# Optimization experiments

Measured on AMD Instinct MI355X. Metric: run time of the kernel, lower is better.

Reference implementation:

```python
import jax, jax.numpy as jnp
import numpy as np

B, N, D = 8, 1024, 256
H = 8
DH = D // H
R = 4          # relation types 0..3; adj value 4 = no relation
FF = 1024
EPS = 1e-5


def _lin(k, fan_in, shape):
    return jax.random.normal(k, shape, jnp.float32) * (1.0 / np.sqrt(fan_in))


def setup_inputs() -> dict:
    key = jax.random.key(0)
    ks = jax.random.split(key, 16)
    src = jax.random.normal(ks[0], (B, N, D), jnp.float32)
    adj_matrix = jax.random.randint(ks[1], (B, N, N), 0, 5, dtype=jnp.int32)
    Wq = _lin(ks[2], D, (D, D)); bq = jnp.zeros((D,), jnp.float32)
    Wk = _lin(ks[3], D, (D, D)); bk = jnp.zeros((D,), jnp.float32)
    Wv = _lin(ks[4], D, (R, D, D)); bv = jnp.zeros((R, D), jnp.float32)
    Wo = _lin(ks[5], D, (D, D)); bo = jnp.zeros((D,), jnp.float32)
    W1 = _lin(ks[6], D, (D, FF)); b1 = jnp.zeros((FF,), jnp.float32)
    W2 = _lin(ks[7], FF, (FF, D)); b2 = jnp.zeros((D,), jnp.float32)
    g1 = jnp.ones((D,), jnp.float32); beta1 = jnp.zeros((D,), jnp.float32)
    g2 = jnp.ones((D,), jnp.float32); beta2 = jnp.zeros((D,), jnp.float32)
    return dict(src=src, adj_matrix=adj_matrix, Wq=Wq, bq=bq, Wk=Wk, bk=bk,
                Wv=Wv, bv=bv, Wo=Wo, bo=bo, W1=W1, b1=b1, W2=W2, b2=b2,
                g1=g1, beta1=beta1, g2=g2, beta2=beta2)


def _ln(x, g, b):
    m = x.mean(-1, keepdims=True)
    v = ((x - m) ** 2).mean(-1, keepdims=True)
    return (x - m) * jax.lax.rsqrt(v + EPS) * g + b


def reference(src, adj_matrix, Wq, bq, Wk, bk, Wv, bv, Wo, bo, W1, b1, W2, b2, g1, beta1, g2, beta2):
    Bb, Nn, Dm = src.shape
    h, dh = H, Dm // H
    q = (src @ Wq + bq).reshape(Bb, Nn, h, dh).transpose(0, 2, 1, 3)  # (B,H,N,dh)
    k = (src @ Wk + bk).reshape(Bb, Nn, h, dh).transpose(0, 2, 1, 3)
    scores = jnp.einsum('bhid,bhjd->bhij', q, k) / np.sqrt(dh)
    attn = jax.nn.softmax(scores, axis=-1)                             # (B,H,N,N)
    out = jnp.zeros_like(q)
    for r in range(Wv.shape[0]):  # small fixed relation loop, matches module
        v_r = (src @ Wv[r] + bv[r]).reshape(Bb, Nn, h, dh).transpose(0, 2, 1, 3)
        mask = (adj_matrix == r)[:, None]                              # (B,1,N,N)
        out = out + jnp.einsum('bhij,bhjd->bhid', attn * mask, v_r)
    attn_out = out.transpose(0, 2, 1, 3).reshape(Bb, Nn, Dm) @ Wo + bo
    x = _ln(src + attn_out, g1, beta1)
    ff = jax.nn.gelu(x @ W1 + b1, approximate=False) @ W2 + b2
    return _ln(x + ff, g2, beta2)
```

## Files before the change

kernel.cpp:

```cpp
#include <hip/hip_runtime.h>
#include <hip/hip_bf16.h>
#include <cmath>

constexpr int CB  = 8;
constexpr int CN  = 1024;
constexpr int CD  = 256;
constexpr int CH  = 8;
constexpr int CDH = 32;
constexpr int CR  = 4;
constexpr int CFF = 1024;
constexpr float CEPS = 1e-5f;
constexpr float CS = 0.25503480f;
constexpr size_t SZH = (size_t)CB * CH * CN * CDH;

#define MODE_QK    0
#define MODE_FFN1  2
#define MODE_VT    4

typedef float v4f __attribute__((ext_vector_type(4)));
typedef short v8s __attribute__((ext_vector_type(8)));

static __device__ __forceinline__ short f2bf(float f) {
    unsigned u = __builtin_bit_cast(unsigned, f);
    u += 0x7fff + ((u >> 16) & 1);
    return (short)(u >> 16);
}
static __device__ __forceinline__ float bf2f(short s) {
    unsigned u = ((unsigned)(unsigned short)s) << 16;
    return __builtin_bit_cast(float, u);
}
static __device__ __forceinline__ unsigned cvtpk_bf16(float lo, float hi) {
    unsigned r;
    asm("v_cvt_pk_bf16_f32 %0, %1, %2" : "=v"(r) : "v"(lo), "v"(hi));
    return r;
}

static __device__ __forceinline__ void async_copy16(const void* g, void* l) {
    __builtin_amdgcn_global_load_lds(
        (const __attribute__((address_space(1))) void*)g,
        (__attribute__((address_space(3))) void*)l, 16, 0, 0);
}


template<int BM, int BN, int MODE>
__device__ __forceinline__ void gemm_body(
    const short* __restrict__ A, const short* __restrict__ Bw,
    const float* __restrict__ biasv, void* __restrict__ dest,
    int M, int K, int Nw, int bx, int by, short* smem)
{
    constexpr int WTM = BM / 2, WTN = BN / 2;
    constexpr int TM = WTM / 16, TN = WTN / 16;
    short* As = smem;
    short* Bs = smem + 2 * BM * 32;

    const int t    = threadIdx.x;
    const int lane = t & 63;
    const int w    = t >> 6;
    const int quad = lane >> 4, l15 = lane & 15;
    const int wm = w >> 1, wn = w & 1;
    const int m0 = bx * BM, n0 = by * BN;

    const int srow = lane >> 2;
    const int scol = (lane & 3) * 8;

    v4f acc[TM][TN];
    #pragma unroll
    for (int i = 0; i < TM; ++i)
        #pragma unroll
        for (int j = 0; j < TN; ++j) acc[i][j] = (v4f){0.f, 0.f, 0.f, 0.f};

    const int NK = K >> 5;

    auto stage = [&](int buf, int kt) {
        #pragma unroll
        for (int u = 0; u < BM / 64; ++u) {
            const int e0 = (w * (BM / 64) + u) * 512;
            const int row = (e0 >> 5) + srow;
            async_copy16(A + (size_t)(m0 + row) * K + kt + scol,
                         &As[buf * BM * 32 + e0]);
        }
        #pragma unroll
        for (int u = 0; u < BN / 64; ++u) {
            const int e0 = (w * (BN / 64) + u) * 512;
            const int row = (e0 >> 5) + srow;
            async_copy16(Bw + (size_t)(n0 + row) * K + kt + scol,
                         &Bs[buf * BN * 32 + e0]);
        }
    };

    stage(0, 0);

    for (int it = 0; it < NK; ++it) {
        __syncthreads();
        if (it + 1 < NK) stage((it + 1) & 1, (it + 1) << 5);

        const int buf = it & 1;
        v8s af[TM], bfr[TN];
        #pragma unroll
        for (int i = 0; i < TM; ++i)
            af[i] = *(const v8s*)&As[buf * BM * 32 +
                                     (wm * WTM + i * 16 + l15) * 32 + quad * 8];
        #pragma unroll
        for (int j = 0; j < TN; ++j)
            bfr[j] = *(const v8s*)&Bs[buf * BN * 32 +
                                      (wn * WTN + j * 16 + l15) * 32 + quad * 8];
        #pragma unroll
        for (int i = 0; i < TM; ++i)
            #pragma unroll
            for (int j = 0; j < TN; ++j)
                acc[i][j] = __builtin_amdgcn_mfma_f32_16x16x32_bf16(
                    af[i], bfr[j], acc[i][j], 0, 0, 0);
    }

    #pragma unroll
    for (int i = 0; i < TM; ++i) {
        #pragma unroll
        for (int j = 0; j < TN; ++j) {
            const int mb = m0 + wm * WTM + i * 16 + quad * 4;
            const int n  = n0 + wn * WTN + j * 16 + l15;
            float vals[4];
            if (MODE == MODE_VT) {
                #pragma unroll
                for (int rr = 0; rr < 4; ++rr) vals[rr] = acc[i][j][rr] + biasv[mb + rr];
            } else {
                #pragma unroll
                for (int rr = 0; rr < 4; ++rr) vals[rr] = acc[i][j][rr] + biasv[n];
            }

            if (MODE == MODE_QK) {
                if (n0 < 256) {
                    #pragma unroll
                    for (int rr = 0; rr < 4; ++rr) vals[rr] *= CS;
                }
                const int b = mb >> 10, ii0 = mb & 1023;
                const int plane = n >> 8, nn = n & 255;
                const int h = nn >> 5, d = nn & 31;
                #pragma unroll
                for (int rr = 0; rr < 4; ++rr)
                    ((short*)dest)[(size_t)plane * SZH +
                        (((size_t)(b * CH + h)) * CN + ii0 + rr) * CDH + d] =
                        f2bf(vals[rr]);
            } else if (MODE == MODE_VT) {
                const int b = n >> 10, ii = n & 1023;
                const int jj = ii & 63;
                const int cc = (((jj >> 4) & 1) << 5) | (((jj >> 2) & 3) << 3) |
                               (((jj >> 5) & 1) << 2) | (jj & 3);
                const int iip = (ii & ~63) | cc;
                #pragma unroll
                for (int rr = 0; rr < 4; ++rr) {
                    const int m = mb + rr;
                    const int r2 = m >> 8, hd = m & 255;
                    const int h = hd >> 5, d = hd & 31;
                    ((short*)dest)[2 * SZH +
                        (((size_t)(r2 * 64 + b * CH + h)) * CDH + d) * CN + iip] =
                        f2bf(vals[rr]);
                }
            } else {
                #pragma unroll
                for (int rr = 0; rr < 4; ++rr) {
                    const size_t idx = (size_t)(mb + rr) * Nw + n;
                    const float xx = vals[rr];
                    const float E = exp2f(2.302217f * (xx + 0.044715f * xx * xx * xx));
                    ((short*)dest)[idx] = f2bf(xx * E / (E + 1.f));
                }
            }
        }
    }
}

template<int BM, int BN, int MODE>
__global__ __launch_bounds__(256)
void gemm_mfma(const short* __restrict__ A, const short* __restrict__ Bw,
               const float* __restrict__ biasv, void* __restrict__ dest,
               int M, int K, int Nw)
{
    extern __shared__ short smem[];
    gemm_body<BM, BN, MODE>(A, Bw, biasv, dest, M, K, Nw,
                            blockIdx.x, blockIdx.y, smem);
}

__global__ __launch_bounds__(256)
void proj_kernel(const short* __restrict__ src_bf, const short* __restrict__ wqkvT,
                 const float* __restrict__ bpack, short* __restrict__ qkv,
                 const int* __restrict__ adj, unsigned char* __restrict__ adj4)
{
    extern __shared__ short smem[];
    const int g = blockIdx.x;
    if (g < 512) {
        gemm_body<64, 128, MODE_QK>(src_bf, wqkvT, bpack, qkv,
                                    8192, 256, 512, g >> 2, g & 3, smem);
    } else if (g < 1536) {
        const int h2 = g - 512;
        gemm_body<64, 128, MODE_VT>(wqkvT + 512 * 256, src_bf, bpack + 512,
                                    qkv, 1024, 256, 8192, h2 & 15, h2 >> 4, smem);
    } else {
        const int nout = CB * CN * CN / 8;
        for (int i = (g - 1536) * 256 + threadIdx.x; i < nout; i += 512 * 256) {
            const int dwi = i & 127;
            const int row = i >> 7;
            const int T   = dwi >> 3, kq = dwi & 7;
            const int j0  = T * 64 + (kq & 3) * 4 + (kq >> 2) * 16;
            const int* p = adj + (size_t)row * CN + j0;
            const int4 q0 = *(const int4*)(p);
            const int4 q1 = *(const int4*)(p + 32);
            const unsigned pk =
                (unsigned)(q0.x & 0xf)         | ((unsigned)(q0.y & 0xf) << 4)  |
                ((unsigned)(q0.z & 0xf) << 8)  | ((unsigned)(q0.w & 0xf) << 12) |
                ((unsigned)(q1.x & 0xf) << 16) | ((unsigned)(q1.y & 0xf) << 20) |
                ((unsigned)(q1.z & 0xf) << 24) | ((unsigned)(q1.w & 0xf) << 28);
            ((unsigned*)adj4)[i] = pk;
        }
    }
}

template<bool OUTF, bool OUTB, bool ADDBF>
__global__ __launch_bounds__(256)
void gemm_ln32(const short* __restrict__ A, const short* __restrict__ Bw,
               const float* __restrict__ biasv, const void* __restrict__ addp,
               const float* __restrict__ gw, const float* __restrict__ be,
               float* __restrict__ outf, short* __restrict__ outb, int K)
{
    __shared__ short As[2][16 * 32];
    __shared__ short Bs[2][256 * 32];
    __shared__ float redS[16][4], redQ[16][4];

    const int t    = threadIdx.x;
    const int lane = t & 63;
    const int w    = t >> 6;
    const int quad = lane >> 4, l15 = lane & 15;
    const int m0   = blockIdx.x * 16;

    const int srow = lane >> 2;
    const int scol = (lane & 3) * 8;

    v4f acc[4];
    #pragma unroll
    for (int j = 0; j < 4; ++j) acc[j] = (v4f){0.f, 0.f, 0.f, 0.f};

    const int NK = K >> 5;

    auto stage = [&](int buf, int kt) {
        if (t < 64)
            async_copy16(A + (size_t)(m0 + (t >> 2)) * K + kt + (t & 3) * 8,
                         &As[buf][t * 8]);
        #pragma unroll
        for (int u = 0; u < 4; ++u) {
            const int e0 = (w * 4 + u) * 512;
            async_copy16(Bw + (size_t)((e0 >> 5) + srow) * K + kt + scol,
                         &Bs[buf][e0]);
        }
    };

    stage(0, 0);

    for (int it = 0; it < NK; ++it) {
        __syncthreads();
        if (it + 1 < NK) stage((it + 1) & 1, (it + 1) << 5);

        const int buf = it & 1;
        const v8s af = *(const v8s*)&As[buf][l15 * 32 + quad * 8];
        #pragma unroll
        for (int j = 0; j < 4; ++j) {
            const v8s bfr = *(const v8s*)&Bs[buf][(w * 64 + 16 * j + l15) * 32 + quad * 8];
            acc[j] = __builtin_amdgcn_mfma_f32_16x16x32_bf16(af, bfr, acc[j], 0, 0, 0);
        }
    }

    float v[4][4];
    #pragma unroll
    for (int rr = 0; rr < 4; ++rr) {
        const int row = m0 + quad * 4 + rr;
        float s = 0.f, sq = 0.f;
        #pragma unroll
        for (int j = 0; j < 4; ++j) {
            const int n = w * 64 + 16 * j + l15;
            const size_t idx = (size_t)row * CD + n;
            const float addv = ADDBF ? bf2f(((const short*)addp)[idx])
                                     : ((const float*)addp)[idx];
            const float x = acc[j][rr] + biasv[n] + addv;
            v[rr][j] = x;
            s += x; sq += x * x;
        }
        #pragma unroll
        for (int off = 1; off < 16; off <<= 1) {
            s  += __shfl_xor(s, off);
            sq += __shfl_xor(sq, off);
        }
        if (l15 == 0) {
            redS[quad * 4 + rr][w] = s;
            redQ[quad * 4 + rr][w] = sq;
        }
    }
    __syncthreads();

    #pragma unroll
    for (int rr = 0; rr < 4; ++rr) {
        const int r16 = quad * 4 + rr;
        const int row = m0 + r16;
        const float s  = (redS[r16][0] + redS[r16][1]) + (redS[r16][2] + redS[r16][3]);
        const float sq = (redQ[r16][0] + redQ[r16][1]) + (redQ[r16][2] + redQ[r16][3]);
        const float mean = s * (1.f / CD);
        const float var  = sq * (1.f / CD) - mean * mean;
        const float rstd = rsqrtf(var + CEPS);
        #pragma unroll
        for (int j = 0; j < 4; ++j) {
            const int n = w * 64 + 16 * j + l15;
            const float y = (v[rr][j] - mean) * rstd * gw[n] + be[n];
            if (OUTF) outf[(size_t)row * CD + n] = y;
            if (OUTB) outb[(size_t)row * CD + n] = f2bf(y);
        }
    }
}

__global__ __launch_bounds__(256)
void prep(const float* __restrict__ src,
          const float* __restrict__ Wq, const float* __restrict__ Wk,
          const float* __restrict__ Wv, const float* __restrict__ Wo,
          const float* __restrict__ W1, const float* __restrict__ W2,
          const float* __restrict__ bq, const float* __restrict__ bk,
          const float* __restrict__ bv, const float* __restrict__ bo,
          const float* __restrict__ b1, const float* __restrict__ b2,
          short* __restrict__ src_bf,
          short* __restrict__ wqkvT, short* __restrict__ woT,
          short* __restrict__ w1T, short* __restrict__ w2T,
          float* __restrict__ bpack)
{
    __shared__ float tile[64][65];
    const int bx = blockIdx.x, t = threadIdx.x;
    if (bx < 2048) {
        const int i = bx * 256 + t;
        const float4 v = ((const float4*)src)[i];
        short4 o;
        o.x = f2bf(v.x); o.y = f2bf(v.y); o.z = f2bf(v.z); o.w = f2bf(v.w);
        ((short4*)src_bf)[i] = o;
    } else if (bx < 2288) {
        const int tt = bx - 2048;
        const float* S; short* D;
        int Sstride, Dstride, k0, srccol, dstrow;
        if (tt < 96) {
            const int tk = tt & 3, tn = tt >> 2;
            const int ng = tn * 64;
            Sstride = 256; Dstride = 256; k0 = tk * 64;
            dstrow = tn * 64; D = wqkvT;
            if (ng < 256)      { S = Wq; srccol = ng; }
            else if (ng < 512) { S = Wk; srccol = ng - 256; }
            else { const int r = (ng - 512) >> 8;
                   S = Wv + (size_t)r * 65536; srccol = (ng - 512) & 255; }
        } else if (tt < 112) {
            const int u = tt - 96, tk = u & 3, tn = u >> 2;
            S = Wo; Sstride = 256; D = woT; Dstride = 256;
            k0 = tk * 64; srccol = tn * 64; dstrow = tn * 64;
        } else if (tt < 176) {
            const int u = tt - 112, tk = u & 3, tn = u >> 2;
            S = W1; Sstride = 1024; D = w1T; Dstride = 256;
            k0 = tk * 64; srccol = tn * 64; dstrow = tn * 64;
        } else {
            const int u = tt - 176, tk = u & 15, tn = u >> 4;
            S = W2; Sstride = 256; D = w2T; Dstride = 1024;
            k0 = tk * 64; srccol = tn * 64; dstrow = tn * 64;
        }
        #pragma unroll
        for (int u2 = 0; u2 < 4; ++u2) {
            const int kl = (t >> 4) + u2 * 16;
            const int nl = (t & 15) * 4;
            const float4 v = *(const float4*)&S[(size_t)(k0 + kl) * Sstride + srccol + nl];
            tile[kl][nl + 0] = v.x; tile[kl][nl + 1] = v.y;
            tile[kl][nl + 2] = v.z; tile[kl][nl + 3] = v.w;
        }
        __syncthreads();
        #pragma unroll
        for (int u2 = 0; u2 < 4; ++u2) {
            const int nl = (t >> 4) + u2 * 16;
            const int kl = (t & 15) * 4;
            short4 o;
            o.x = f2bf(tile[kl + 0][nl]); o.y = f2bf(tile[kl + 1][nl]);
            o.z = f2bf(tile[kl + 2][nl]); o.w = f2bf(tile[kl + 3][nl]);
            *(short4*)&D[(size_t)(dstrow + nl) * Dstride + k0 + kl] = o;
        }
    } else {
        const int idx = (bx - 2288) * 256 + t;
        float bvv;
        if (idx < 256)       bvv = bq[idx];
        else if (idx < 512)  bvv = bk[idx - 256];
        else if (idx < 1536) bvv = bv[idx - 512];
        else if (idx < 1792) bvv = bo[idx - 1536];
        else if (idx < 2816) bvv = b1[idx - 1792];
        else                 bvv = b2[idx - 2816];
        bpack[idx] = bvv;
    }
}

__global__ __launch_bounds__(256, 4)
void attn_mfma(const short* __restrict__ qg, const short* __restrict__ kg,
               const short* __restrict__ vt, const unsigned char* __restrict__ adj4,
               short* __restrict__ outh)
{
    __shared__ __align__(16) short vtl[2][8192];

    const int t    = threadIdx.x;
    const int lane = t & 63;
    const int w    = t >> 6;
    const int quad = lane >> 4;
    const int l15  = lane & 15;
    const int g    = blockIdx.x;
    const int b    = g & 7;
    const int h    = (g >> 3) & 7;
    const int i0   = (g >> 6) * 64;
    const int bhh  = b * CH + h;
    const size_t bh = (size_t)bhh;

    const v8s qfrag = *(const v8s*)&qg[(bh * CN + i0 + 16 * w + l15) * CDH + quad * 8];

    const short* vsrc[4];
    #pragma unroll
    for (int u = 0; u < 4; ++u) {
        const int gl = t + 256 * u;
        const int r = gl >> 8, d = (gl >> 3) & 31, gc = gl & 7;
        vsrc[u] = vt + ((size_t)(r * 64 + bhh) * CDH + d) * CN + (gc ^ (d & 7)) * 8;
    }
    const short* kbase = kg + (bh * CN + l15) * CDH + quad * 8;
    const unsigned char* abase =
        adj4 + ((size_t)(b * CN) + i0 + 16 * w + l15) * (CN / 2) + quad * 4;

    v4f oacc[2];
    oacc[0] = (v4f){0.f, 0.f, 0.f, 0.f};
    oacc[1] = (v4f){0.f, 0.f, 0.f, 0.f};
    float plsum = 0.f;
    const int psw = (l15 & 7) * 8;

    #pragma unroll
    for (int u = 0; u < 4; ++u)
        async_copy16(vsrc[u], &vtl[0][(t + 256 * u) * 8]);
    v8s kpre[4];
    #pragma unroll
    for (int jb = 0; jb < 4; ++jb)
        kpre[jb] = *(const v8s*)(kbase + (16 * jb) * CDH);
    unsigned apre0 = *(const unsigned*)(abase);
    unsigned apre1 = *(const unsigned*)(abase + 16);

    for (int jt = 0; jt < 16; ++jt) {
        __syncthreads();
        const int p = jt & 1;

        v4f sacc[4];
        #pragma unroll
        for (int jb = 0; jb < 4; ++jb)
            sacc[jb] = __builtin_amdgcn_mfma_f32_16x16x32_bf16(
                kpre[jb], qfrag, (v4f){0.f, 0.f, 0.f, 0.f}, 0, 0, 0);

        const unsigned a0 = apre0, a1 = apre1;
        const int jn = (jt + 1) & 15;
        #pragma unroll
        for (int u = 0; u < 4; ++u)
            async_copy16(vsrc[u] + jn * 64, &vtl[p ^ 1][(t + 256 * u) * 8]);
        #pragma unroll
        for (int jb = 0; jb < 4; ++jb)
            kpre[jb] = *(const v8s*)(kbase + (jn * 64 + 16 * jb) * CDH);
        apre0 = *(const unsigned*)(abase + jn * 32);
        apre1 = *(const unsigned*)(abase + jn * 32 + 16);

        float pv[4][4];
        #pragma unroll
        for (int jb = 0; jb < 4; ++jb)
            #pragma unroll
            for (int rr = 0; rr < 4; ++rr) pv[jb][rr] = exp2f(sacc[jb][rr]);
        plsum += ((pv[0][0] + pv[0][1]) + (pv[0][2] + pv[0][3]))
               + ((pv[1][0] + pv[1][1]) + (pv[1][2] + pv[1][3]))
               + ((pv[2][0] + pv[2][1]) + (pv[2][2] + pv[2][3]))
               + ((pv[3][0] + pv[3][1]) + (pv[3][2] + pv[3][3]));

        #pragma unroll
        for (int kb = 0; kb < 2; ++kb) {
            const unsigned P[4] = {
                cvtpk_bf16(pv[kb][0],     pv[kb][1]),
                cvtpk_bf16(pv[kb][2],     pv[kb][3]),
                cvtpk_bf16(pv[kb + 2][0], pv[kb + 2][1]),
                cvtpk_bf16(pv[kb + 2][2], pv[kb + 2][3])};
            const unsigned ab32 = kb ? a1 : a0;
            unsigned pf[4][4];
            #pragma unroll
            for (int u = 0; u < 4; ++u) {
                const unsigned sel = 0x0c000c00u | (unsigned)u | ((unsigned)u << 16);
                const unsigned a2 = __builtin_amdgcn_perm(ab32, ab32, sel) & 0x00F0000Fu;
                #pragma unroll
                for (int r = 0; r < 4; ++r) {
                    const unsigned x = a2 ^ ((unsigned)r | ((unsigned)r << 20));
                    unsigned tt, mm;
                    asm("v_pk_add_i16 %0, %1, %2"
                        : "=v"(tt) : "v"(x), "v"(0xffffffffu));
                    asm("v_pk_ashrrev_i16 %0, %1, %2"
                        : "=v"(mm) : "v"(0x000f000fu), "v"(tt));
                    pf[r][u] = P[u] & mm;
                }
            }
            #pragma unroll
            for (int r = 0; r < 4; ++r) {
                const v8s pfr = __builtin_bit_cast(v8s,
                    make_uint4(pf[r][0], pf[r][1], pf[r][2], pf[r][3]));
                #pragma unroll
                for (int cb = 0; cb < 2; ++cb) {
                    const v8s vfrag = *(const v8s*)&vtl[p][r * 2048 +
                        (16 * cb + l15) * 64 + (((4 * kb + quad) * 8) ^ psw)];
                    oacc[cb] = __builtin_amdgcn_mfma_f32_16x16x32_bf16(
                        pfr, vfrag, oacc[cb], 0, 0, 0);
                }
            }
        }
    }

    float plF = plsum;
    plF += __shfl_xor(plF, 16);
    plF += __shfl_xor(plF, 32);
    #pragma unroll
    for (int rr = 0; rr < 4; ++rr) {
        const float inv = 1.f / __shfl(plF, quad * 4 + rr);
        const int row = i0 + 16 * w + quad * 4 + rr;
        #pragma unroll
        for (int cb = 0; cb < 2; ++cb)
            outh[((size_t)b * CN + row) * CD + h * CDH + 16 * cb + l15] =
                f2bf(oacc[cb][rr] * inv);
    }
}

extern "C" void kernel_launch(void* const* d_in, const int* in_sizes, int n_in,
                              void* d_out, int out_size, void* d_ws, size_t ws_size,
                              hipStream_t stream)
{
    const float* src = (const float*)d_in[0];
    const int*   adj = (const int*)d_in[1];
    const float* Wq  = (const float*)d_in[2];
    const float* bq  = (const float*)d_in[3];
    const float* Wk  = (const float*)d_in[4];
    const float* bk  = (const float*)d_in[5];
    const float* Wv  = (const float*)d_in[6];
    const float* bv  = (const float*)d_in[7];
    const float* Wo  = (const float*)d_in[8];
    const float* bo  = (const float*)d_in[9];
    const float* W1  = (const float*)d_in[10];
    const float* b1  = (const float*)d_in[11];
    const float* W2  = (const float*)d_in[12];
    const float* b2  = (const float*)d_in[13];
    const float* g1  = (const float*)d_in[14];
    const float* be1 = (const float*)d_in[15];
    const float* g2  = (const float*)d_in[16];
    const float* be2 = (const float*)d_in[17];
    float* out = (float*)d_out;

    char* wsb = (char*)d_ws;
    const size_t MB = (size_t)1 << 20;

    unsigned char* adj4 = (unsigned char*)(wsb);
    short* qkv_bf = (short*)(wsb + 8 * MB);
    short* src_bf = (short*)(wsb + 32 * MB);
    short* wqkvT  = (short*)(wsb + 36 * MB);
    short* woT    = (short*)(wsb + 36 * MB + 768 * 1024);
    short* w1T    = (short*)(wsb + 36 * MB + 896 * 1024);
    short* w2T    = (short*)(wsb + 36 * MB + 1408 * 1024);
    float* bpack  = (float*)(wsb + 36 * MB + 1920 * 1024);
    short* heads_bf = (short*)(wsb + 38 * MB);
    short* x_bf   = (short*)(wsb + 32 * MB);
    short* h1_bf  = (short*)(wsb + 16 * MB);

    const int M = CB * CN;
    dim3 blk(256);

    prep<<<dim3(2300), blk, 0, stream>>>(src, Wq, Wk, Wv, Wo, W1, W2,
        bq, bk, bv, bo, b1, b2, src_bf, wqkvT, woT, w1T, w2T, bpack);

    proj_kernel<<<dim3(2048), blk, 24576, stream>>>(
        src_bf, wqkvT, bpack, qkv_bf, adj, adj4);

    attn_mfma<<<dim3(1024), blk, 0, stream>>>(
        qkv_bf, qkv_bf + SZH, qkv_bf + 2 * SZH, adj4, heads_bf);

    gemm_ln32<false, true, false><<<dim3(M / 16), blk, 0, stream>>>(
        heads_bf, woT, bpack + 1536, src, g1, be1, nullptr, x_bf, CD);

    gemm_mfma<64, 128, MODE_FFN1><<<dim3(M / 64, CFF / 128), blk, 24576, stream>>>(
        x_bf, w1T, bpack + 1792, h1_bf, M, CD, CFF);

    gemm_ln32<true, false, true><<<dim3(M / 16), blk, 0, stream>>>(
        h1_bf, w2T, bpack + 2816, x_bf, g2, be2, out, nullptr, CFF);
}
```

Measured before the change: 228.7 us.

## Store adjacency as bytes with perm-based masks and use 128x128 GEMM tiles

The packed adjacency changes from 4-bit nibbles to one byte per entry. The attention kernel now builds the per-relation bf16 masks with a few v_perm lookups instead of packed-int16 add/shift sequences, which cuts ALU work in the inner loop. The cost is twice the adjacency bytes written by proj_kernel and read in attention (8 MB instead of 4 MB). Separately, the QK, VT and FFN1 GEMMs move from 64x128 to 128x128 tiles, giving fewer blocks with more LDS each.

```diff
diff --git a/kernel.cpp b/kernel.cpp
--- a/kernel.cpp
+++ b/kernel.cpp
@@ -182,20 +182,20 @@
 __global__ __launch_bounds__(256)
 void proj_kernel(const short* __restrict__ src_bf, const short* __restrict__ wqkvT,
                  const float* __restrict__ bpack, short* __restrict__ qkv,
-                 const int* __restrict__ adj, unsigned char* __restrict__ adj4)
+                 const int* __restrict__ adj, unsigned char* __restrict__ adjsel)
 {
     extern __shared__ short smem[];
     const int g = blockIdx.x;
-    if (g < 512) {
-        gemm_body<64, 128, MODE_QK>(src_bf, wqkvT, bpack, qkv,
-                                    8192, 256, 512, g >> 2, g & 3, smem);
-    } else if (g < 1536) {
-        const int h2 = g - 512;
-        gemm_body<64, 128, MODE_VT>(wqkvT + 512 * 256, src_bf, bpack + 512,
-                                    qkv, 1024, 256, 8192, h2 & 15, h2 >> 4, smem);
+    if (g < 256) {
+        gemm_body<128, 128, MODE_QK>(src_bf, wqkvT, bpack, qkv,
+                                     8192, 256, 512, g >> 2, g & 3, smem);
+    } else if (g < 768) {
+        const int h2 = g - 256;
+        gemm_body<128, 128, MODE_VT>(wqkvT + 512 * 256, src_bf, bpack + 512,
+                                     qkv, 1024, 256, 8192, h2 & 7, h2 >> 3, smem);
     } else {
         const int nout = CB * CN * CN / 8;
-        for (int i = (g - 1536) * 256 + threadIdx.x; i < nout; i += 512 * 256) {
+        for (int i = (g - 768) * 256 + threadIdx.x; i < nout; i += 512 * 256) {
             const int dwi = i & 127;
             const int row = i >> 7;
             const int T   = dwi >> 3, kq = dwi & 7;
@@ -203,12 +203,12 @@
             const int* p = adj + (size_t)row * CN + j0;
             const int4 q0 = *(const int4*)(p);
             const int4 q1 = *(const int4*)(p + 32);
-            const unsigned pk =
-                (unsigned)(q0.x & 0xf)         | ((unsigned)(q0.y & 0xf) << 4)  |
-                ((unsigned)(q0.z & 0xf) << 8)  | ((unsigned)(q0.w & 0xf) << 12) |
-                ((unsigned)(q1.x & 0xf) << 16) | ((unsigned)(q1.y & 0xf) << 20) |
-                ((unsigned)(q1.z & 0xf) << 24) | ((unsigned)(q1.w & 0xf) << 28);
-            ((unsigned*)adj4)[i] = pk;
+            int2 o;
+            o.x = (q0.x & 0xff) | ((q0.y & 0xff) << 8) |
+                  ((q0.z & 0xff) << 16) | ((q0.w & 0xff) << 24);
+            o.y = (q1.x & 0xff) | ((q1.y & 0xff) << 8) |
+                  ((q1.z & 0xff) << 16) | ((q1.w & 0xff) << 24);
+            ((int2*)adjsel)[i] = o;
         }
     }
 }
@@ -392,7 +392,7 @@
 
 __global__ __launch_bounds__(256, 4)
 void attn_mfma(const short* __restrict__ qg, const short* __restrict__ kg,
-               const short* __restrict__ vt, const unsigned char* __restrict__ adj4,
+               const short* __restrict__ vt, const unsigned char* __restrict__ adjsel,
                short* __restrict__ outh)
 {
     __shared__ __align__(16) short vtl[2][8192];
@@ -420,7 +420,7 @@
     }
     const short* kbase = kg + (bh * CN + l15) * CDH + quad * 8;
     const unsigned char* abase =
-        adj4 + ((size_t)(b * CN) + i0 + 16 * w + l15) * (CN / 2) + quad * 4;
+        adjsel + ((size_t)(b * CN) + i0 + 16 * w + l15) * CN + quad * 8;
 
     v4f oacc[2];
     oacc[0] = (v4f){0.f, 0.f, 0.f, 0.f};
@@ -435,8 +435,8 @@
     #pragma unroll
     for (int jb = 0; jb < 4; ++jb)
         kpre[jb] = *(const v8s*)(kbase + (16 * jb) * CDH);
-    unsigned apre0 = *(const unsigned*)(abase);
-    unsigned apre1 = *(const unsigned*)(abase + 16);
+    int2 apre0 = *(const int2*)(abase);
+    int2 apre1 = *(const int2*)(abase + 32);
 
     for (int jt = 0; jt < 16; ++jt) {
         __syncthreads();
@@ -448,7 +448,7 @@
             sacc[jb] = __builtin_amdgcn_mfma_f32_16x16x32_bf16(
                 kpre[jb], qfrag, (v4f){0.f, 0.f, 0.f, 0.f}, 0, 0, 0);
 
-        const unsigned a0 = apre0, a1 = apre1;
+        const int2 a0 = apre0, a1 = apre1;
         const int jn = (jt + 1) & 15;
         #pragma unroll
         for (int u = 0; u < 4; ++u)
@@ -456,8 +456,8 @@
         #pragma unroll
         for (int jb = 0; jb < 4; ++jb)
             kpre[jb] = *(const v8s*)(kbase + (jn * 64 + 16 * jb) * CDH);
-        apre0 = *(const unsigned*)(abase + jn * 32);
-        apre1 = *(const unsigned*)(abase + jn * 32 + 16);
+        apre0 = *(const int2*)(abase + jn * 64);
+        apre1 = *(const int2*)(abase + jn * 64 + 32);
 
         float pv[4][4];
         #pragma unroll
@@ -476,27 +476,21 @@
                 cvtpk_bf16(pv[kb][2],     pv[kb][3]),
                 cvtpk_bf16(pv[kb + 2][0], pv[kb + 2][1]),
                 cvtpk_bf16(pv[kb + 2][2], pv[kb + 2][3])};
-            const unsigned ab32 = kb ? a1 : a0;
-            unsigned pf[4][4];
-            #pragma unroll
-            for (int u = 0; u < 4; ++u) {
-                const unsigned sel = 0x0c000c00u | (unsigned)u | ((unsigned)u << 16);
-                const unsigned a2 = __builtin_amdgcn_perm(ab32, ab32, sel) & 0x00F0000Fu;
-                #pragma unroll
-                for (int r = 0; r < 4; ++r) {
-                    const unsigned x = a2 ^ ((unsigned)r | ((unsigned)r << 20));
-                    unsigned tt, mm;
-                    asm("v_pk_add_i16 %0, %1, %2"
-                        : "=v"(tt) : "v"(x), "v"(0xffffffffu));
-                    asm("v_pk_ashrrev_i16 %0, %1, %2"
-                        : "=v"(mm) : "v"(0x000f000fu), "v"(tt));
-                    pf[r][u] = P[u] & mm;
-                }
-            }
+            const int2 aa = kb ? a1 : a0;
+            const unsigned D[4] = {
+                __builtin_amdgcn_perm((unsigned)aa.x, (unsigned)aa.x, 0x01010000u),
+                __builtin_amdgcn_perm((unsigned)aa.x, (unsigned)aa.x, 0x03030202u),
+                __builtin_amdgcn_perm((unsigned)aa.y, (unsigned)aa.y, 0x01010000u),
+                __builtin_amdgcn_perm((unsigned)aa.y, (unsigned)aa.y, 0x03030202u)};
             #pragma unroll
             for (int r = 0; r < 4; ++r) {
+                const unsigned tb = 0xffu << (8 * r);
+                unsigned pf[4];
+                #pragma unroll
+                for (int u = 0; u < 4; ++u)
+                    pf[u] = P[u] & __builtin_amdgcn_perm(0u, tb, D[u]);
                 const v8s pfr = __builtin_bit_cast(v8s,
-                    make_uint4(pf[r][0], pf[r][1], pf[r][2], pf[r][3]));
+                    make_uint4(pf[0], pf[1], pf[2], pf[3]));
                 #pragma unroll
                 for (int cb = 0; cb < 2; ++cb) {
                     const v8s vfrag = *(const v8s*)&vtl[p][r * 2048 +
@@ -549,7 +543,7 @@
     char* wsb = (char*)d_ws;
     const size_t MB = (size_t)1 << 20;
 
-    unsigned char* adj4 = (unsigned char*)(wsb);
+    unsigned char* adjsel = (unsigned char*)(wsb);
     short* qkv_bf = (short*)(wsb + 8 * MB);
     short* src_bf = (short*)(wsb + 32 * MB);
     short* wqkvT  = (short*)(wsb + 36 * MB);
@@ -567,16 +561,16 @@
     prep<<<dim3(2300), blk, 0, stream>>>(src, Wq, Wk, Wv, Wo, W1, W2,
         bq, bk, bv, bo, b1, b2, src_bf, wqkvT, woT, w1T, w2T, bpack);
 
-    proj_kernel<<<dim3(2048), blk, 24576, stream>>>(
-        src_bf, wqkvT, bpack, qkv_bf, adj, adj4);
+    proj_kernel<<<dim3(1280), blk, 32768, stream>>>(
+        src_bf, wqkvT, bpack, qkv_bf, adj, adjsel);
 
     attn_mfma<<<dim3(1024), blk, 0, stream>>>(
-        qkv_bf, qkv_bf + SZH, qkv_bf + 2 * SZH, adj4, heads_bf);
+        qkv_bf, qkv_bf + SZH, qkv_bf + 2 * SZH, adjsel, heads_bf);
 
     gemm_ln32<false, true, false><<<dim3(M / 16), blk, 0, stream>>>(
         heads_bf, woT, bpack + 1536, src, g1, be1, nullptr, x_bf, CD);
 
-    gemm_mfma<64, 128, MODE_FFN1><<<dim3(M / 64, CFF / 128), blk, 24576, stream>>>(
+    gemm_mfma<128, 128, MODE_FFN1><<<dim3(M / 128, CFF / 128), blk, 32768, stream>>>(
         x_bf, w1T, bpack + 1792, h1_bf, M, CD, CFF);
 
     gemm_ln32<true, false, true><<<dim3(M / 16), blk, 0, stream>>>(
```

Result: no change. 225.6 us (-1.3%).
